# Kernel optimization log

Measured on AMD Instinct MI355X. Metric: run time of the kernel, lower is better.

Reference implementation:

```python
import jax, jax.numpy as jnp
import numpy as np

EPS = 1e-7  # K.epsilon()
ROUTINGS = 3

def squash(v, axis=-1):
    s2 = jnp.sum(jnp.square(v), axis=axis, keepdims=True)
    scale = s2 / (1.0 + s2) / jnp.sqrt(s2 + EPS)
    return scale * v

def setup_inputs() -> dict:
    key = jax.random.key(0)
    k1, k2 = jax.random.split(key)
    B, N, I = 128, 512, 256   # batch, input_num_capsule, input_dim_capsule
    M, D = 32, 16             # num_capsule, dim_capsule
    x = jax.random.normal(k1, (B, N, I), dtype=jnp.float32)
    W = jax.random.normal(k2, (M, N, D, I), dtype=jnp.float32) * 0.05
    return {"x": x, "W": W}

def reference(x, W):
    # x: [B,N,I], W: [M,N,D,I]
    # inputs_hat[b,m,n,d] = sum_i x[b,n,i] * W[m,n,d,i]
    inputs_hat = jnp.einsum('bni,mndi->bmnd', x, W)
    B, M, N, _ = inputs_hat.shape
    b = jnp.zeros((B, M, N), dtype=inputs_hat.dtype)
    outputs = None
    for i in range(ROUTINGS):
        c = jax.nn.softmax(b, axis=1)  # softmax over num_capsule dim (dim=1)
        s = jnp.einsum('bmn,bmnd->bmd', c, inputs_hat)
        outputs = squash(s)
        if i < ROUTINGS - 1:
            b = b + jnp.einsum('bmd,bmnd->bmn', outputs, inputs_hat)
    return outputs
```

## Files before the change

kernel.cpp:

```cpp
#include <hip/hip_runtime.h>
#include <stdint.h>

#define B_ 128
#define N_ 512
#define I_ 256
#define M_ 32
#define D_ 16

typedef __attribute__((ext_vector_type(4))) float f32x4;
typedef __attribute__((ext_vector_type(4))) float float4v;
typedef __attribute__((ext_vector_type(8))) short short8;
typedef __attribute__((ext_vector_type(4))) unsigned int u32x4;
typedef __attribute__((ext_vector_type(4))) unsigned short ushort4v;
typedef unsigned short ushort;

__device__ __forceinline__ float bf2f(ushort u) {
    union { unsigned int i; float f; } v; v.i = ((unsigned int)u) << 16; return v.f;
}
__device__ __forceinline__ ushort f2bf(float f) {
    union { float f; unsigned int i; } v; v.f = f;
    unsigned int r = v.i + 0x7FFFu + ((v.i >> 16) & 1u);
    return (ushort)(r >> 16);
}

__device__ __forceinline__ short8 cvt8(float4v lo, float4v hi) {
    unsigned int u0, u1, u2, u3;
    asm("v_cvt_pk_bf16_f32 %0, %1, %2" : "=v"(u0) : "v"(lo[0]), "v"(lo[1]));
    asm("v_cvt_pk_bf16_f32 %0, %1, %2" : "=v"(u1) : "v"(lo[2]), "v"(lo[3]));
    asm("v_cvt_pk_bf16_f32 %0, %1, %2" : "=v"(u2) : "v"(hi[0]), "v"(hi[1]));
    asm("v_cvt_pk_bf16_f32 %0, %1, %2" : "=v"(u3) : "v"(hi[2]), "v"(hi[3]));
    u32x4 uv = {u0, u1, u2, u3};
    return __builtin_bit_cast(short8, uv);
}

#define GL16(dst, base, imm) \
    asm volatile("global_load_dwordx4 %0, %1, off offset:%2" \
                 : "=&v"(dst) : "v"(base), "n"(imm))

#define VMW(nn) do { \
    asm volatile("s_waitcnt vmcnt(" #nn ")" ::: "memory"); \
    __builtin_amdgcn_sched_barrier(0); \
} while (0)

__global__ __launch_bounds__(512, 4) void hat_gemm(const float* __restrict__ x,
                                                   const float* __restrict__ W,
                                                   ushort* __restrict__ hat) {
    __shared__ ushort As[128 * 256];

    const int bid = blockIdx.x;
    const int n   = (bid & 7) * 64 + (bid >> 3);

    const int tid  = threadIdx.x;
    const int lane = tid & 63;
    const int w    = tid >> 6;
    const int l15  = lane & 15;
    const int kq   = lane >> 4;

    {
        const int row = tid >> 2;
        const int seg = tid & 3;
        const float* xp = x + ((size_t)row * N_ + n) * I_ + seg * 64;
        float4v sv[16];
        #pragma unroll
        for (int j = 0; j < 16; ++j) GL16(sv[j], xp, j * 16);
        VMW(0);
        #pragma unroll
        for (int i = 0; i < 8; ++i) {
            short8 h = cvt8(sv[2 * i], sv[2 * i + 1]);
            const int gsw = ((seg * 8 + i) ^ (row & 15));
            *(short8*)&As[row * 256 + gsw * 8] = h;
        }
    }
    __syncthreads();

    const int abase = l15 * 256;

    #pragma unroll
    for (int mq = 0; mq < 4; ++mq) {
        const int m = w * 4 + mq;
        const float* wb = W + (((size_t)m * N_ + n) * D_ + l15) * I_ + kq * 8;

        f32x4 acc[8];
        #pragma unroll
        for (int a = 0; a < 8; ++a) { f32x4 z = {0.f, 0.f, 0.f, 0.f}; acc[a] = z; }

        float4v L0, H0, L1, H1;
        GL16(L0, wb, 0);   GL16(H0, wb, 16);
        GL16(L1, wb, 128); GL16(H1, wb, 144);

        #pragma unroll
        for (int ks = 0; ks < 8; ++ks) {
            if (ks < 7) VMW(2); else VMW(0);
            short8 bb;
            if ((ks & 1) == 0) bb = cvt8(L0, H0); else bb = cvt8(L1, H1);
            if (ks < 6) {
                const int off = (ks + 2) * 128;
                if ((ks & 1) == 0) { GL16(L0, wb, off); GL16(H0, wb, off + 16); }
                else               { GL16(L1, wb, off); GL16(H1, wb, off + 16); }
            }
            const int gsw = ((ks * 4 + kq) ^ l15) * 8;
            #pragma unroll
            for (int a = 0; a < 8; ++a) {
                short8 af = *(const short8*)&As[abase + a * 4096 + gsw];
                acc[a] = __builtin_amdgcn_mfma_f32_16x16x32_bf16(af, bb, acc[a], 0, 0, 0);
            }
        }

        #pragma unroll
        for (int a = 0; a < 8; ++a) {
            #pragma unroll
            for (int r = 0; r < 4; ++r) {
                const int brow = a * 16 + kq * 4 + r;
                const size_t idx = (((size_t)brow * M_ + m) * N_ + n) * D_ + l15;
                hat[idx] = f2bf(acc[a][r]);
            }
        }
    }
}

__global__ __launch_bounds__(512) void routing(const ushort* __restrict__ hat,
                                               float* __restrict__ out) {
    __shared__ float blog[M_][N_];
    __shared__ float cmax[N_];
    __shared__ float rcsum[N_];

    const int b    = blockIdx.x;
    const int tid  = threadIdx.x;
    const int lane = tid & 63;
    const int w    = tid >> 6;

    #pragma unroll
    for (int m = 0; m < M_; ++m) blog[m][tid] = 0.f;
    __syncthreads();

    float ov[4][16];

    for (int it = 0; it < 3; ++it) {
        {
            float mx = -3.4e38f;
            #pragma unroll
            for (int m = 0; m < M_; ++m) mx = fmaxf(mx, blog[m][tid]);
            float s = 0.f;
            #pragma unroll
            for (int m = 0; m < M_; ++m) s += __expf(blog[m][tid] - mx);
            cmax[tid]  = mx;
            rcsum[tid] = 1.f / s;
        }
        __syncthreads();

        float sacc[4][16];
        #pragma unroll
        for (int q = 0; q < 4; ++q)
            #pragma unroll
            for (int dd = 0; dd < 16; ++dd) sacc[q][dd] = 0.f;

        for (int r = 0; r < 8; ++r) {
            const int nn = r * 64 + lane;
            #pragma unroll
            for (int q = 0; q < 4; ++q) {
                const int m = w * 4 + q;
                const float cm = __expf(blog[m][nn] - cmax[nn]) * rcsum[nn];
                const size_t base = (((size_t)b * M_ + m) * N_ + nn) * D_;
                short8 h0 = *(const short8*)(hat + base);
                short8 h1 = *(const short8*)(hat + base + 8);
                #pragma unroll
                for (int dd = 0; dd < 8; ++dd) {
                    sacc[q][dd]     += cm * bf2f((ushort)h0[dd]);
                    sacc[q][8 + dd] += cm * bf2f((ushort)h1[dd]);
                }
            }
        }
        #pragma unroll
        for (int off = 32; off >= 1; off >>= 1) {
            #pragma unroll
            for (int q = 0; q < 4; ++q)
                #pragma unroll
                for (int dd = 0; dd < 16; ++dd)
                    sacc[q][dd] += __shfl_xor(sacc[q][dd], off, 64);
        }
        #pragma unroll
        for (int q = 0; q < 4; ++q) {
            float s2 = 0.f;
            #pragma unroll
            for (int dd = 0; dd < 16; ++dd) s2 += sacc[q][dd] * sacc[q][dd];
            const float scale = s2 / (1.f + s2) / sqrtf(s2 + 1e-7f);
            #pragma unroll
            for (int dd = 0; dd < 16; ++dd) ov[q][dd] = scale * sacc[q][dd];
        }

        if (it < 2) {
            for (int r = 0; r < 8; ++r) {
                const int nn = r * 64 + lane;
                #pragma unroll
                for (int q = 0; q < 4; ++q) {
                    const int m = w * 4 + q;
                    const size_t base = (((size_t)b * M_ + m) * N_ + nn) * D_;
                    short8 h0 = *(const short8*)(hat + base);
                    short8 h1 = *(const short8*)(hat + base + 8);
                    float dot = 0.f;
                    #pragma unroll
                    for (int dd = 0; dd < 8; ++dd) {
                        dot += ov[q][dd]     * bf2f((ushort)h0[dd]);
                        dot += ov[q][8 + dd] * bf2f((ushort)h1[dd]);
                    }
                    blog[m][nn] += dot;
                }
            }
        }
        __syncthreads();
    }

    if (lane == 0) {
        #pragma unroll
        for (int q = 0; q < 4; ++q) {
            const int m = w * 4 + q;
            #pragma unroll
            for (int c4 = 0; c4 < 4; ++c4) {
                float4v v;
                v[0] = ov[q][c4 * 4 + 0];
                v[1] = ov[q][c4 * 4 + 1];
                v[2] = ov[q][c4 * 4 + 2];
                v[3] = ov[q][c4 * 4 + 3];
                *(float4v*)&out[((size_t)b * M_ + m) * D_ + c4 * 4] = v;
            }
        }
    }
}

extern "C" void kernel_launch(void* const* d_in, const int* in_sizes, int n_in,
                              void* d_out, int out_size, void* d_ws, size_t ws_size,
                              hipStream_t stream) {
    const float* x = (const float*)d_in[0];
    const float* W = (const float*)d_in[1];
    ushort* hat = (ushort*)d_ws;
    float* out = (float*)d_out;

    hat_gemm<<<dim3(N_), dim3(512), 0, stream>>>(x, W, hat);
    routing<<<dim3(B_), dim3(512), 0, stream>>>(hat, out);
}
```

Measured before the change: 173.8 us.

## Stage W through double-buffered LDS with coalesced loads; keep x fragments in registers

```diff
diff --git a/kernel.cpp b/kernel.cpp
--- a/kernel.cpp
+++ b/kernel.cpp
@@ -10,8 +10,8 @@
 typedef __attribute__((ext_vector_type(4))) float f32x4;
 typedef __attribute__((ext_vector_type(4))) float float4v;
 typedef __attribute__((ext_vector_type(8))) short short8;
+typedef __attribute__((ext_vector_type(2))) unsigned int u32x2;
 typedef __attribute__((ext_vector_type(4))) unsigned int u32x4;
-typedef __attribute__((ext_vector_type(4))) unsigned short ushort4v;
 typedef unsigned short ushort;
 
 __device__ __forceinline__ float bf2f(ushort u) {
@@ -32,20 +32,27 @@
     u32x4 uv = {u0, u1, u2, u3};
     return __builtin_bit_cast(short8, uv);
 }
+__device__ __forceinline__ u32x2 cvt4(float4v v) {
+    unsigned int u0, u1;
+    asm("v_cvt_pk_bf16_f32 %0, %1, %2" : "=v"(u0) : "v"(v[0]), "v"(v[1]));
+    asm("v_cvt_pk_bf16_f32 %0, %1, %2" : "=v"(u1) : "v"(v[2]), "v"(v[3]));
+    u32x2 r = {u0, u1};
+    return r;
+}
 
 #define GL16(dst, base, imm) \
     asm volatile("global_load_dwordx4 %0, %1, off offset:%2" \
                  : "=&v"(dst) : "v"(base), "n"(imm))
 
-#define VMW(nn) do { \
-    asm volatile("s_waitcnt vmcnt(" #nn ")" ::: "memory"); \
+#define VMW0() do { \
+    asm volatile("s_waitcnt vmcnt(0)" ::: "memory"); \
     __builtin_amdgcn_sched_barrier(0); \
 } while (0)
 
-__global__ __launch_bounds__(512, 4) void hat_gemm(const float* __restrict__ x,
+__global__ __launch_bounds__(512, 2) void hat_gemm(const float* __restrict__ x,
                                                    const float* __restrict__ W,
                                                    ushort* __restrict__ hat) {
-    __shared__ ushort As[128 * 256];
+    __shared__ ushort LDS[32768];
 
     const int bid = blockIdx.x;
     const int n   = (bid & 7) * 64 + (bid >> 3);
@@ -60,62 +67,79 @@
         const int row = tid >> 2;
         const int seg = tid & 3;
         const float* xp = x + ((size_t)row * N_ + n) * I_ + seg * 64;
-        float4v sv[16];
-        #pragma unroll
-        for (int j = 0; j < 16; ++j) GL16(sv[j], xp, j * 16);
-        VMW(0);
+        float4v sx[16];
+        #pragma unroll
+        for (int j = 0; j < 16; ++j) GL16(sx[j], xp, j * 16);
+        VMW0();
         #pragma unroll
         for (int i = 0; i < 8; ++i) {
-            short8 h = cvt8(sv[2 * i], sv[2 * i + 1]);
-            const int gsw = ((seg * 8 + i) ^ (row & 15));
-            *(short8*)&As[row * 256 + gsw * 8] = h;
-        }
-    }
-    __syncthreads();
-
-    const int abase = l15 * 256;
-
+            short8 h = cvt8(sx[2 * i], sx[2 * i + 1]);
+            const int gsw = (seg * 8 + i) ^ (row & 15);
+            *(short8*)&LDS[row * 256 + gsw * 8] = h;
+        }
+    }
+    __syncthreads();
+
+    short8 afr[8];
     #pragma unroll
-    for (int mq = 0; mq < 4; ++mq) {
-        const int m = w * 4 + mq;
-        const float* wb = W + (((size_t)m * N_ + n) * D_ + l15) * I_ + kq * 8;
-
-        f32x4 acc[8];
-        #pragma unroll
-        for (int a = 0; a < 8; ++a) { f32x4 z = {0.f, 0.f, 0.f, 0.f}; acc[a] = z; }
-
-        float4v L0, H0, L1, H1;
-        GL16(L0, wb, 0);   GL16(H0, wb, 16);
-        GL16(L1, wb, 128); GL16(H1, wb, 144);
-
-        #pragma unroll
-        for (int ks = 0; ks < 8; ++ks) {
-            if (ks < 7) VMW(2); else VMW(0);
-            short8 bb;
-            if ((ks & 1) == 0) bb = cvt8(L0, H0); else bb = cvt8(L1, H1);
-            if (ks < 6) {
-                const int off = (ks + 2) * 128;
-                if ((ks & 1) == 0) { GL16(L0, wb, off); GL16(H0, wb, off + 16); }
-                else               { GL16(L1, wb, off); GL16(H1, wb, off + 16); }
-            }
-            const int gsw = ((ks * 4 + kq) ^ l15) * 8;
-            #pragma unroll
-            for (int a = 0; a < 8; ++a) {
-                short8 af = *(const short8*)&As[abase + a * 4096 + gsw];
-                acc[a] = __builtin_amdgcn_mfma_f32_16x16x32_bf16(af, bb, acc[a], 0, 0, 0);
-            }
-        }
-
-        #pragma unroll
-        for (int a = 0; a < 8; ++a) {
+    for (int ks = 0; ks < 8; ++ks)
+        afr[ks] = *(const short8*)&LDS[(w * 16 + l15) * 256 + (((ks * 4 + kq) ^ l15) * 8)];
+
+    float4v sv[8];
+
+    #define ISSUEW(c) do { \
+        _Pragma("unroll") \
+        for (int u = 0; u < 8; ++u) { \
+            const int rr = w * 8 + u;           \
+            const int ml = rr >> 4, dd = rr & 15; \
+            const float* wp = W + ((((size_t)((c) * 4 + ml)) * N_ + n) * D_ + dd) * I_ + lane * 4; \
+            GL16(sv[u], wp, 0); \
+        } \
+    } while (0)
+
+    #define WRITEW(c) do { \
+        ushort* buf = &LDS[((c) & 1) * 16384]; \
+        _Pragma("unroll") \
+        for (int u = 0; u < 8; ++u) { \
+            const int rr = w * 8 + u; \
+            const int dd = rr & 15; \
+            u32x2 h = cvt4(sv[u]); \
+            *(u32x2*)&buf[rr * 256 + (((lane >> 1) ^ dd) * 8) + (lane & 1) * 4] = h; \
+        } \
+    } while (0)
+
+    ISSUEW(0);
+    __syncthreads();
+    VMW0();
+    WRITEW(0);
+    __syncthreads();
+
+    for (int c = 0; c < 8; ++c) {
+        if (c < 7) ISSUEW(c + 1);
+        const ushort* buf = &LDS[(c & 1) * 16384];
+        #pragma unroll
+        for (int mq = 0; mq < 4; ++mq) {
+            const int m = c * 4 + mq;
+            f32x4 acc = {0.f, 0.f, 0.f, 0.f};
+            #pragma unroll
+            for (int ks = 0; ks < 8; ++ks) {
+                short8 bf = *(const short8*)&buf[(mq * 16 + l15) * 256 + (((ks * 4 + kq) ^ l15) * 8)];
+                acc = __builtin_amdgcn_mfma_f32_16x16x32_bf16(afr[ks], bf, acc, 0, 0, 0);
+            }
             #pragma unroll
             for (int r = 0; r < 4; ++r) {
-                const int brow = a * 16 + kq * 4 + r;
-                const size_t idx = (((size_t)brow * M_ + m) * N_ + n) * D_ + l15;
-                hat[idx] = f2bf(acc[a][r]);
-            }
-        }
-    }
+                const int b = w * 16 + kq * 4 + r;
+                hat[(((size_t)b * M_ + m) * N_ + n) * D_ + l15] = f2bf(acc[r]);
+            }
+        }
+        if (c < 7) {
+            VMW0();
+            WRITEW(c + 1);
+            __syncthreads();
+        }
+    }
+    #undef ISSUEW
+    #undef WRITEW
 }
 
 __global__ __launch_bounds__(512) void routing(const ushort* __restrict__ hat,
@@ -134,6 +158,7 @@
     __syncthreads();
 
     float ov[4][16];
+    typedef __attribute__((ext_vector_type(4))) float fl4;
 
     for (int it = 0; it < 3; ++it) {
         {
@@ -216,12 +241,12 @@
             const int m = w * 4 + q;
             #pragma unroll
             for (int c4 = 0; c4 < 4; ++c4) {
-                float4v v;
+                fl4 v;
                 v[0] = ov[q][c4 * 4 + 0];
                 v[1] = ov[q][c4 * 4 + 1];
                 v[2] = ov[q][c4 * 4 + 2];
                 v[3] = ov[q][c4 * 4 + 3];
-                *(float4v*)&out[((size_t)b * M_ + m) * D_ + c4 * 4] = v;
+                *(fl4*)&out[((size_t)b * M_ + m) * D_ + c4 * 4] = v;
             }
         }
     }
```

Result: faster. 161.3 us (-7.2%).
